# Optimization experiments

Hardware: AMD Instinct MI355X
Metric: run time of the kernel (lower is better)

Reference implementation:

```python
import jax, jax.numpy as jnp
import numpy as np

EMBED_DIM = 1024
BATCH, SEQ = 4, 2048


def setup_inputs() -> dict:
    key = jax.random.key(0)
    k1, k2 = jax.random.split(key)
    hidden_states = jax.random.normal(k1, (BATCH, SEQ, EMBED_DIM), dtype=jnp.float32)
    # fused QKV projection weight (Linear(embed_dim, 3*embed_dim, bias=False)),
    # stored as [E, 3E] so y = x @ W
    W_qkv = jax.random.normal(k2, (EMBED_DIM, 3 * EMBED_DIM), dtype=jnp.float32) * (1.0 / np.sqrt(EMBED_DIM))
    return {"hidden_states": hidden_states, "W_qkv": W_qkv}


def reference(hidden_states, W_qkv):
    E = hidden_states.shape[-1]
    scale = 1.0 / np.sqrt(E)
    qkv = jnp.einsum('bse,ef->bsf', hidden_states, W_qkv)  # [B,S,3E]
    q, k, v = jnp.split(qkv, 3, axis=-1)                   # each [B,S,E]
    # scores = q @ (k^T * scale); softmax over keys
    scores = jnp.einsum('bqe,bke->bqk', q, k) * scale      # [B,S,S]
    w = jax.nn.softmax(scores, axis=-1)
    return jnp.einsum('bqk,bke->bqe', w, v)                # [B,S,E]
```

## Files before the change

### kernel.cpp

```cpp
#include <hip/hip_runtime.h>

typedef __attribute__((ext_vector_type(8))) short short8;
typedef __attribute__((ext_vector_type(8))) unsigned short ushort8;
typedef __attribute__((ext_vector_type(4))) float f32x4;

__device__ __forceinline__ float bf2f(unsigned short u) {
  union { unsigned int u; float f; } c; c.u = ((unsigned int)u) << 16; return c.f;
}
__device__ __forceinline__ unsigned short f2bf(float f) {
  union { float f; unsigned int u; } c; c.f = f;
  unsigned int x = c.u;
  return (unsigned short)((x + 0x7FFFu + ((x >> 16) & 1u)) >> 16);
}

#define GLD_LDS16(g, l)                                                        \
  __builtin_amdgcn_global_load_lds(                                            \
      (const __attribute__((address_space(1))) void*)(g),                      \
      (__attribute__((address_space(3))) void*)(l), 16, 0, 0)

__global__ __launch_bounds__(256) void prep_kernel(
    const float* __restrict__ X, unsigned short* __restrict__ Xb,
    const float* __restrict__ W, unsigned short* __restrict__ Wt,
    float* __restrict__ Lrow) {
  const int t = threadIdx.x;
  if (blockIdx.x < 4096) {
    long i = ((long)blockIdx.x * 256 + t) * 8;
    float4 a = *(const float4*)(X + i);
    float4 b = *(const float4*)(X + i + 4);
    ushort8 o;
    o[0] = f2bf(a.x); o[1] = f2bf(a.y); o[2] = f2bf(a.z); o[3] = f2bf(a.w);
    o[4] = f2bf(b.x); o[5] = f2bf(b.y); o[6] = f2bf(b.z); o[7] = f2bf(b.w);
    *(ushort8*)(Xb + i) = o;
  } else if (blockIdx.x < 4864) {
    const int bid = blockIdx.x - 4096;
    const int f0 = (bid % 48) * 64;
    const int e0 = (bid / 48) * 64;
    __shared__ unsigned short tile[64][65];
    const int cg = (t & 15) * 4;
    const int r = t >> 4;
#pragma unroll
    for (int i = 0; i < 4; ++i) {
      int e = r + i * 16;
      float4 v = *(const float4*)(W + (long)(e0 + e) * 3072 + f0 + cg);
      tile[e][cg + 0] = f2bf(v.x);
      tile[e][cg + 1] = f2bf(v.y);
      tile[e][cg + 2] = f2bf(v.z);
      tile[e][cg + 3] = f2bf(v.w);
    }
    __syncthreads();
#pragma unroll
    for (int i = 0; i < 4; ++i) {
      int f = (t >> 4) + i * 16;
      int e = (t & 15) * 4;
      ushort4 o;
      o.x = tile[e + 0][f];
      o.y = tile[e + 1][f];
      o.z = tile[e + 2][f];
      o.w = tile[e + 3][f];
      *(ushort4*)(Wt + (long)(f0 + f) * 1024 + e0 + e) = o;
    }
  } else {
    float4 z = {0.f, 0.f, 0.f, 0.f};
#pragma unroll
    for (int j = 0; j < 8; ++j) *(float4*)(Lrow + (j * 256 + t) * 4) = z;
  }
}

template <int MODE>
__device__ __forceinline__ void gemm_body(
    const unsigned short* __restrict__ A, const unsigned short* __restrict__ B,
    void* __restrict__ Cv, int K, int lda, int ldb, int ldc,
    long sA, long sB, long sC, float alpha, float* __restrict__ Lrow,
    unsigned short* __restrict__ Vt) {
  constexpr int BM = 128, BN = 128, BK = 64;
  __shared__ __align__(16) unsigned short smem[BM * BK + BN * BK];
  unsigned short* As = smem;
  unsigned short* Bs = smem + BM * BK;

  const int t = threadIdx.x;
  const int lane = t & 63;
  const int wave = t >> 6;
  const int quad = lane >> 4;
  const int mrow = lane & 15;
  const int wm = wave >> 1, wn = wave & 1;

  const int bx = blockIdx.x, by = blockIdx.y;
  const int rowA0 = by * BM;
  const int rowB0 = bx * BN;
  const int b = blockIdx.z;
  const unsigned short* Ab = A + (long)b * sA;
  const unsigned short* Bb = B + (long)b * sB;

  f32x4 acc[4][4];
#pragma unroll
  for (int i = 0; i < 4; ++i)
#pragma unroll
    for (int j = 0; j < 4; ++j) {
      f32x4 z = {0.f, 0.f, 0.f, 0.f};
      acc[i][j] = z;
    }

  const int rbase = wave * 32 + (lane >> 3);
  const int c2 = lane & 7;

  for (int kt = 0; kt < K; kt += BK) {
#pragma unroll
    for (int j = 0; j < 4; ++j) {
      int r = rbase + j * 8;
      int c = c2 ^ (r & 7);
      GLD_LDS16(Ab + (long)(rowA0 + r) * lda + kt + c * 8, As + (wave * 4 + j) * 512);
      GLD_LDS16(Bb + (long)(rowB0 + r) * ldb + kt + c * 8, Bs + (wave * 4 + j) * 512);
    }
    __syncthreads();
#pragma unroll
    for (int ks = 0; ks < 2; ++ks) {
      short8 af[4], bfr[4];
#pragma unroll
      for (int i = 0; i < 4; ++i) {
        int rA = wm * 64 + i * 16 + mrow;
        int cc = ks * 4 + quad;
        af[i] = *(const short8*)(As + (rA * 8 + (cc ^ (rA & 7))) * 8);
        int rB = wn * 64 + i * 16 + mrow;
        bfr[i] = *(const short8*)(Bs + (rB * 8 + (cc ^ (rB & 7))) * 8);
      }
#pragma unroll
      for (int mt = 0; mt < 4; ++mt)
#pragma unroll
        for (int nt = 0; nt < 4; ++nt)
          acc[mt][nt] = __builtin_amdgcn_mfma_f32_16x16x32_bf16(
              af[mt], bfr[nt], acc[mt][nt], 0, 0, 0);
    }
    __syncthreads();
  }

  const int m_base = rowA0 + wm * 64;
  const int n_base = rowB0 + wn * 64;
  const long cb = (long)b * sC;

  if constexpr (MODE == 0) {
    if (bx < 16) {
#pragma unroll
      for (int mt = 0; mt < 4; ++mt)
#pragma unroll
        for (int nt = 0; nt < 4; ++nt)
#pragma unroll
          for (int i = 0; i < 4; ++i) {
            int row = m_base + mt * 16 + quad * 4 + i;
            int col = n_base + nt * 16 + mrow;
            ((unsigned short*)Cv)[cb + (long)row * ldc + col] = f2bf(acc[mt][nt][i]);
          }
    } else {
#pragma unroll
      for (int mt = 0; mt < 4; ++mt)
#pragma unroll
        for (int nt = 0; nt < 4; ++nt) {
          int r4 = wm * 64 + mt * 16 + quad * 4;
          int cL = wn * 64 + nt * 16 + mrow;
          int swz = ((cL & 7) << 4) ^ (((cL >> 3) & 3) << 3);
          ushort4 pk;
          pk.x = f2bf(acc[mt][nt][0]);
          pk.y = f2bf(acc[mt][nt][1]);
          pk.z = f2bf(acc[mt][nt][2]);
          pk.w = f2bf(acc[mt][nt][3]);
          *(ushort4*)(smem + cL * 128 + (r4 ^ swz)) = pk;
        }
      __syncthreads();
      const int batch = by >> 4;
      const int s_base = (by & 15) * 128;
      const int e_base = (bx - 16) * 128;
      unsigned short* VtB = Vt + (long)batch * 1024 * 2048;
#pragma unroll
      for (int rnd = 0; rnd < 8; ++rnd) {
        int e = (t >> 4) + rnd * 16;
        int s = (t & 15) * 8;
        int swz = ((e & 7) << 4) ^ (((e >> 3) & 3) << 3);
        ushort8 v = *(const ushort8*)(smem + e * 128 + (s ^ swz));
        *(ushort8*)(VtB + (long)(e_base + e) * 2048 + s_base + s) = v;
      }
    }
  } else if constexpr (MODE == 1) {
    float p[4][4];
#pragma unroll
    for (int mt = 0; mt < 4; ++mt)
#pragma unroll
      for (int i = 0; i < 4; ++i) p[mt][i] = 0.f;
#pragma unroll
    for (int mt = 0; mt < 4; ++mt)
#pragma unroll
      for (int nt = 0; nt < 4; ++nt)
#pragma unroll
        for (int i = 0; i < 4; ++i) {
          int row = m_base + mt * 16 + quad * 4 + i;
          int col = n_base + nt * 16 + mrow;
          float e = __expf(acc[mt][nt][i] * alpha);
          ((unsigned short*)Cv)[cb + (long)row * ldc + col] = f2bf(e);
          p[mt][i] += e;
        }
#pragma unroll
    for (int off = 1; off < 16; off <<= 1)
#pragma unroll
      for (int mt = 0; mt < 4; ++mt)
#pragma unroll
        for (int i = 0; i < 4; ++i)
          p[mt][i] += __shfl_xor(p[mt][i], off, 64);
    if (mrow == 0) {
#pragma unroll
      for (int mt = 0; mt < 4; ++mt)
#pragma unroll
        for (int i = 0; i < 4; ++i) {
          int row = m_base + mt * 16 + quad * 4 + i;
          atomicAdd(&Lrow[b * 2048 + row], p[mt][i]);
        }
    }
  } else {
#pragma unroll
    for (int mt = 0; mt < 4; ++mt)
#pragma unroll
      for (int i = 0; i < 4; ++i) {
        int row = m_base + mt * 16 + quad * 4 + i;
        float inv = 1.0f / Lrow[b * 2048 + row];
#pragma unroll
        for (int nt = 0; nt < 4; ++nt) {
          int col = n_base + nt * 16 + mrow;
          ((float*)Cv)[cb + (long)row * ldc + col] = acc[mt][nt][i] * inv;
        }
      }
  }
}

__global__ __launch_bounds__(256, 2) void qkv_gemm_kernel(
    const unsigned short* __restrict__ A, const unsigned short* __restrict__ B,
    void* __restrict__ Cv, int K, int lda, int ldb, int ldc,
    long sA, long sB, long sC, float alpha, float* __restrict__ Lrow,
    unsigned short* __restrict__ Vt) {
  gemm_body<0>(A, B, Cv, K, lda, ldb, ldc, sA, sB, sC, alpha, Lrow, Vt);
}
__global__ __launch_bounds__(256, 2) void score_gemm_kernel(
    const unsigned short* __restrict__ A, const unsigned short* __restrict__ B,
    void* __restrict__ Cv, int K, int lda, int ldb, int ldc,
    long sA, long sB, long sC, float alpha, float* __restrict__ Lrow,
    unsigned short* __restrict__ Vt) {
  gemm_body<1>(A, B, Cv, K, lda, ldb, ldc, sA, sB, sC, alpha, Lrow, Vt);
}
__global__ __launch_bounds__(256, 2) void out_gemm_kernel(
    const unsigned short* __restrict__ A, const unsigned short* __restrict__ B,
    void* __restrict__ Cv, int K, int lda, int ldb, int ldc,
    long sA, long sB, long sC, float alpha, float* __restrict__ Lrow,
    unsigned short* __restrict__ Vt) {
  gemm_body<2>(A, B, Cv, K, lda, ldb, ldc, sA, sB, sC, alpha, Lrow, Vt);
}

extern "C" void kernel_launch(void* const* d_in, const int* in_sizes, int n_in,
                              void* d_out, int out_size, void* d_ws, size_t ws_size,
                              hipStream_t stream) {
  const float* X = (const float*)d_in[0];
  const float* W = (const float*)d_in[1];
  float* out = (float*)d_out;

  char* ws = (char*)d_ws;
  unsigned short* Xb  = (unsigned short*)(ws);
  unsigned short* Wtb = (unsigned short*)(ws + 16777216);
  unsigned short* QK  = (unsigned short*)(ws + 23068672);
  unsigned short* Vt  = (unsigned short*)(ws + 56623104);
  unsigned short* Sb  = (unsigned short*)(ws + 73400320);
  float* Lrow         = (float*)(ws + 106954752);

  prep_kernel<<<4865, 256, 0, stream>>>(X, Xb, W, Wtb, Lrow);

  qkv_gemm_kernel<<<dim3(24, 64, 1), 256, 0, stream>>>(
      Xb, Wtb, QK, 1024, 1024, 1024, 2048, 0L, 0L, 0L, 1.0f, nullptr, Vt);

  score_gemm_kernel<<<dim3(16, 16, 4), 256, 0, stream>>>(
      QK, QK + 1024, Sb, 1024, 2048, 2048, 2048,
      (long)2048 * 2048, (long)2048 * 2048, (long)2048 * 2048, 0.03125f, Lrow, nullptr);

  out_gemm_kernel<<<dim3(8, 16, 4), 256, 0, stream>>>(
      Sb, Vt, out, 2048, 2048, 2048, 1024,
      (long)2048 * 2048, (long)1024 * 2048, (long)2048 * 1024, 1.0f, Lrow, nullptr);
}
```

Baseline: 228.8 us.

## Add 256x256-tile 8-wave pipelined GEMM for QKV and score kernels

Introduces a new GEMM body with 256x256 output tiles, 512 threads (8 waves), a double-buffered LDS pipeline of direct global-to-LDS loads split into half-K phases, raw barriers, and setprio around MFMA bursts. The QKV projection and score GEMMs switch to this body with smaller grids; the output GEMM keeps the old 128x128 body. The larger tiles raise data reuse and cut global traffic, and the interleaved loads try to hide memory latency behind MFMAs. In exchange it uses 128KB of LDS and many accumulator registers per block, so occupancy drops and the score grid becomes only 256 blocks, which may underfill the GPU.

```diff
diff --git a/kernel.cpp b/kernel.cpp
--- a/kernel.cpp
+++ b/kernel.cpp
@@ -17,6 +17,12 @@
   __builtin_amdgcn_global_load_lds(                                            \
       (const __attribute__((address_space(1))) void*)(g),                      \
       (__attribute__((address_space(3))) void*)(l), 16, 0, 0)
+
+__device__ __forceinline__ void bar() {
+  asm volatile("" ::: "memory");
+  __builtin_amdgcn_s_barrier();
+  asm volatile("" ::: "memory");
+}
 
 __global__ __launch_bounds__(256) void prep_kernel(
     const float* __restrict__ X, unsigned short* __restrict__ Xb,
@@ -67,6 +73,242 @@
 }
 
 template <int MODE>
+__device__ __forceinline__ void gemm256_body(
+    const unsigned short* __restrict__ A, const unsigned short* __restrict__ B,
+    void* __restrict__ Cv, int K, int lda, int ldb, int ldc,
+    long sA, long sB, long sC, float alpha, float* __restrict__ Lrow,
+    unsigned short* __restrict__ Vt) {
+  __shared__ __align__(16) unsigned short smem[65536];
+
+  const int t = threadIdx.x;
+  const int lane = t & 63;
+  const int wave = t >> 6;
+  const int quad = lane >> 4;
+  const int mrow = lane & 15;
+  const int wm = wave >> 2;
+  const int wn = wave & 3;
+
+  const int bx = blockIdx.x, by = blockIdx.y, b = blockIdx.z;
+  const int rowA0 = by * 256;
+  const int rowB0 = bx * 256;
+  const unsigned short* Ab = A + (long)b * sA;
+  const unsigned short* Bb = B + (long)b * sB;
+
+  const int srow = lane >> 2;
+  const int schunk = (lane & 3) * 8;
+
+  f32x4 acc[8][4];
+#pragma unroll
+  for (int i = 0; i < 8; ++i)
+#pragma unroll
+    for (int j = 0; j < 4; ++j) {
+      f32x4 z = {0.f, 0.f, 0.f, 0.f};
+      acc[i][j] = z;
+    }
+
+  const int NT = K >> 6;
+
+  auto stg = [&](const unsigned short* gb, int ld, int r0, int kt, int kh,
+                 int roff) {
+#pragma unroll
+    for (int j = 0; j < 2; ++j)
+      GLD_LDS16(gb + (long)(r0 + j * 128 + wave * 16 + srow) * ld + kt +
+                    kh * 32 + schunk,
+                smem + roff + (j * 128 + wave * 16) * 32);
+  };
+
+  stg(Ab, lda, rowA0, 0, 0, 0);
+  stg(Bb, ldb, rowB0, 0, 0, 16384);
+  stg(Ab, lda, rowA0, 0, 1, 8192);
+  stg(Bb, ldb, rowB0, 0, 1, 24576);
+  stg(Bb, ldb, rowB0, 64, 0, 32768 + 16384);
+  stg(Ab, lda, rowA0, 64, 0, 32768);
+  asm volatile("s_waitcnt vmcnt(4)" ::: "memory");
+  bar();
+
+  const int rA_base = wm * 128 + mrow;
+  const int rB_base = wn * 64 + mrow;
+  const int qoff = quad * 8;
+
+  for (int T = 0; T < NT; ++T) {
+    const int buf = (T & 1) << 15;
+    const int nbuf = buf ^ 32768;
+    const unsigned short* A0 = smem + buf;
+    const unsigned short* A1 = smem + buf + 8192;
+    const unsigned short* B0 = smem + buf + 16384;
+    const unsigned short* B1 = smem + buf + 24576;
+    const int ktn = (T + 1) << 6;
+    const int ktn2 = (T + 2) << 6;
+    short8 af[4], bf[4];
+
+#pragma unroll
+    for (int i = 0; i < 4; ++i)
+      af[i] = *(const short8*)(A0 + (rA_base + i * 16) * 32 + qoff);
+#pragma unroll
+    for (int j = 0; j < 4; ++j)
+      bf[j] = *(const short8*)(B0 + (rB_base + j * 16) * 32 + qoff);
+    if (T + 1 < NT) stg(Ab, lda, rowA0, ktn, 1, nbuf + 8192);
+    bar();
+    __builtin_amdgcn_sched_barrier(0);
+    __builtin_amdgcn_s_setprio(1);
+#pragma unroll
+    for (int i = 0; i < 4; ++i)
+#pragma unroll
+      for (int j = 0; j < 4; ++j)
+        acc[i][j] = __builtin_amdgcn_mfma_f32_16x16x32_bf16(af[i], bf[j],
+                                                            acc[i][j], 0, 0, 0);
+    __builtin_amdgcn_s_setprio(0);
+    __builtin_amdgcn_sched_barrier(0);
+    bar();
+
+#pragma unroll
+    for (int i = 0; i < 4; ++i)
+      af[i] = *(const short8*)(A0 + (rA_base + 64 + i * 16) * 32 + qoff);
+    if (T + 1 < NT) stg(Bb, ldb, rowB0, ktn, 1, nbuf + 24576);
+    bar();
+    __builtin_amdgcn_sched_barrier(0);
+    __builtin_amdgcn_s_setprio(1);
+#pragma unroll
+    for (int i = 0; i < 4; ++i)
+#pragma unroll
+      for (int j = 0; j < 4; ++j)
+        acc[4 + i][j] = __builtin_amdgcn_mfma_f32_16x16x32_bf16(
+            af[i], bf[j], acc[4 + i][j], 0, 0, 0);
+    __builtin_amdgcn_s_setprio(0);
+    __builtin_amdgcn_sched_barrier(0);
+    bar();
+
+#pragma unroll
+    for (int i = 0; i < 4; ++i)
+      af[i] = *(const short8*)(A1 + (rA_base + i * 16) * 32 + qoff);
+#pragma unroll
+    for (int j = 0; j < 4; ++j)
+      bf[j] = *(const short8*)(B1 + (rB_base + j * 16) * 32 + qoff);
+    if (T + 2 < NT) stg(Bb, ldb, rowB0, ktn2, 0, buf + 16384);
+    bar();
+    __builtin_amdgcn_sched_barrier(0);
+    __builtin_amdgcn_s_setprio(1);
+#pragma unroll
+    for (int i = 0; i < 4; ++i)
+#pragma unroll
+      for (int j = 0; j < 4; ++j)
+        acc[i][j] = __builtin_amdgcn_mfma_f32_16x16x32_bf16(af[i], bf[j],
+                                                            acc[i][j], 0, 0, 0);
+    __builtin_amdgcn_s_setprio(0);
+    __builtin_amdgcn_sched_barrier(0);
+    bar();
+
+#pragma unroll
+    for (int i = 0; i < 4; ++i)
+      af[i] = *(const short8*)(A1 + (rA_base + 64 + i * 16) * 32 + qoff);
+    if (T + 2 < NT) stg(Ab, lda, rowA0, ktn2, 0, buf);
+    bar();
+    __builtin_amdgcn_sched_barrier(0);
+    __builtin_amdgcn_s_setprio(1);
+#pragma unroll
+    for (int i = 0; i < 4; ++i)
+#pragma unroll
+      for (int j = 0; j < 4; ++j)
+        acc[4 + i][j] = __builtin_amdgcn_mfma_f32_16x16x32_bf16(
+            af[i], bf[j], acc[4 + i][j], 0, 0, 0);
+    __builtin_amdgcn_s_setprio(0);
+    __builtin_amdgcn_sched_barrier(0);
+    if (T + 2 < NT) {
+      asm volatile("s_waitcnt vmcnt(4)" ::: "memory");
+    } else if (T + 1 < NT) {
+      asm volatile("s_waitcnt vmcnt(0)" ::: "memory");
+    }
+    bar();
+  }
+
+  const long cb = (long)b * sC;
+
+  if constexpr (MODE == 0) {
+    if (bx < 8) {
+      unsigned short* C = (unsigned short*)Cv;
+#pragma unroll
+      for (int m = 0; m < 8; ++m) {
+        int row = rowA0 + wm * 128 + m * 16 + quad * 4;
+#pragma unroll
+        for (int j = 0; j < 4; ++j) {
+          int col = rowB0 + wn * 64 + j * 16 + mrow;
+#pragma unroll
+          for (int r = 0; r < 4; ++r)
+            C[(long)(row + r) * ldc + col] = f2bf(acc[m][j][r]);
+        }
+      }
+    } else {
+#pragma unroll
+      for (int m = 0; m < 8; ++m) {
+        int s4 = wm * 128 + m * 16 + quad * 4;
+#pragma unroll
+        for (int j = 0; j < 4; ++j) {
+          int e = wn * 64 + j * 16 + mrow;
+          int swz = ((e & 7) << 4) ^ (((e >> 3) & 3) << 3);
+          ushort4 pk;
+          pk.x = f2bf(acc[m][j][0]);
+          pk.y = f2bf(acc[m][j][1]);
+          pk.z = f2bf(acc[m][j][2]);
+          pk.w = f2bf(acc[m][j][3]);
+          *(ushort4*)(smem + e * 256 + (s4 ^ swz)) = pk;
+        }
+      }
+      __syncthreads();
+      const int batch = by >> 3;
+      const int s_base = (by & 7) * 256;
+      const int e_base = (bx - 8) * 256;
+      unsigned short* VtB = Vt + (long)batch * 1024 * 2048;
+      const int er = t >> 5;
+      const int s = (t & 31) * 8;
+#pragma unroll
+      for (int rnd = 0; rnd < 16; ++rnd) {
+        int e = rnd * 16 + er;
+        int swz = ((e & 7) << 4) ^ (((e >> 3) & 3) << 3);
+        ushort8 v = *(const ushort8*)(smem + e * 256 + (s ^ swz));
+        *(ushort8*)(VtB + (long)(e_base + e) * 2048 + s_base + s) = v;
+      }
+    }
+  } else {
+    unsigned short* C = (unsigned short*)Cv;
+    float p[8][4];
+#pragma unroll
+    for (int m = 0; m < 8; ++m)
+#pragma unroll
+      for (int r = 0; r < 4; ++r) p[m][r] = 0.f;
+#pragma unroll
+    for (int m = 0; m < 8; ++m) {
+      int row = rowA0 + wm * 128 + m * 16 + quad * 4;
+#pragma unroll
+      for (int j = 0; j < 4; ++j) {
+        int col = rowB0 + wn * 64 + j * 16 + mrow;
+#pragma unroll
+        for (int r = 0; r < 4; ++r) {
+          float e = __expf(acc[m][j][r] * alpha);
+          C[cb + (long)(row + r) * ldc + col] = f2bf(e);
+          p[m][r] += e;
+        }
+      }
+    }
+#pragma unroll
+    for (int off = 1; off < 16; off <<= 1)
+#pragma unroll
+      for (int m = 0; m < 8; ++m)
+#pragma unroll
+        for (int r = 0; r < 4; ++r)
+          p[m][r] += __shfl_xor(p[m][r], off, 64);
+    if (mrow == 0) {
+#pragma unroll
+      for (int m = 0; m < 8; ++m) {
+        int row = rowA0 + wm * 128 + m * 16 + quad * 4;
+#pragma unroll
+        for (int r = 0; r < 4; ++r)
+          atomicAdd(&Lrow[b * 2048 + row + r], p[m][r]);
+      }
+    }
+  }
+}
+
+template <int MODE>
 __device__ __forceinline__ void gemm_body(
     const unsigned short* __restrict__ A, const unsigned short* __restrict__ B,
     void* __restrict__ Cv, int K, int lda, int ldb, int ldc,
@@ -137,110 +379,33 @@
   const int n_base = rowB0 + wn * 64;
   const long cb = (long)b * sC;
 
-  if constexpr (MODE == 0) {
-    if (bx < 16) {
-#pragma unroll
-      for (int mt = 0; mt < 4; ++mt)
-#pragma unroll
-        for (int nt = 0; nt < 4; ++nt)
-#pragma unroll
-          for (int i = 0; i < 4; ++i) {
-            int row = m_base + mt * 16 + quad * 4 + i;
-            int col = n_base + nt * 16 + mrow;
-            ((unsigned short*)Cv)[cb + (long)row * ldc + col] = f2bf(acc[mt][nt][i]);
-          }
-    } else {
-#pragma unroll
-      for (int mt = 0; mt < 4; ++mt)
-#pragma unroll
-        for (int nt = 0; nt < 4; ++nt) {
-          int r4 = wm * 64 + mt * 16 + quad * 4;
-          int cL = wn * 64 + nt * 16 + mrow;
-          int swz = ((cL & 7) << 4) ^ (((cL >> 3) & 3) << 3);
-          ushort4 pk;
-          pk.x = f2bf(acc[mt][nt][0]);
-          pk.y = f2bf(acc[mt][nt][1]);
-          pk.z = f2bf(acc[mt][nt][2]);
-          pk.w = f2bf(acc[mt][nt][3]);
-          *(ushort4*)(smem + cL * 128 + (r4 ^ swz)) = pk;
-        }
-      __syncthreads();
-      const int batch = by >> 4;
-      const int s_base = (by & 15) * 128;
-      const int e_base = (bx - 16) * 128;
-      unsigned short* VtB = Vt + (long)batch * 1024 * 2048;
-#pragma unroll
-      for (int rnd = 0; rnd < 8; ++rnd) {
-        int e = (t >> 4) + rnd * 16;
-        int s = (t & 15) * 8;
-        int swz = ((e & 7) << 4) ^ (((e >> 3) & 3) << 3);
-        ushort8 v = *(const ushort8*)(smem + e * 128 + (s ^ swz));
-        *(ushort8*)(VtB + (long)(e_base + e) * 2048 + s_base + s) = v;
-      }
-    }
-  } else if constexpr (MODE == 1) {
-    float p[4][4];
-#pragma unroll
-    for (int mt = 0; mt < 4; ++mt)
-#pragma unroll
-      for (int i = 0; i < 4; ++i) p[mt][i] = 0.f;
-#pragma unroll
-    for (int mt = 0; mt < 4; ++mt)
-#pragma unroll
-      for (int nt = 0; nt < 4; ++nt)
-#pragma unroll
-        for (int i = 0; i < 4; ++i) {
-          int row = m_base + mt * 16 + quad * 4 + i;
-          int col = n_base + nt * 16 + mrow;
-          float e = __expf(acc[mt][nt][i] * alpha);
-          ((unsigned short*)Cv)[cb + (long)row * ldc + col] = f2bf(e);
-          p[mt][i] += e;
-        }
-#pragma unroll
-    for (int off = 1; off < 16; off <<= 1)
-#pragma unroll
-      for (int mt = 0; mt < 4; ++mt)
-#pragma unroll
-        for (int i = 0; i < 4; ++i)
-          p[mt][i] += __shfl_xor(p[mt][i], off, 64);
-    if (mrow == 0) {
-#pragma unroll
-      for (int mt = 0; mt < 4; ++mt)
-#pragma unroll
-        for (int i = 0; i < 4; ++i) {
-          int row = m_base + mt * 16 + quad * 4 + i;
-          atomicAdd(&Lrow[b * 2048 + row], p[mt][i]);
-        }
-    }
-  } else {
-#pragma unroll
-    for (int mt = 0; mt < 4; ++mt)
-#pragma unroll
-      for (int i = 0; i < 4; ++i) {
-        int row = m_base + mt * 16 + quad * 4 + i;
-        float inv = 1.0f / Lrow[b * 2048 + row];
-#pragma unroll
-        for (int nt = 0; nt < 4; ++nt) {
-          int col = n_base + nt * 16 + mrow;
-          ((float*)Cv)[cb + (long)row * ldc + col] = acc[mt][nt][i] * inv;
-        }
-      }
-  }
-}
-
-__global__ __launch_bounds__(256, 2) void qkv_gemm_kernel(
+#pragma unroll
+  for (int mt = 0; mt < 4; ++mt)
+#pragma unroll
+    for (int i = 0; i < 4; ++i) {
+      int row = m_base + mt * 16 + quad * 4 + i;
+      float inv = 1.0f / Lrow[b * 2048 + row];
+#pragma unroll
+      for (int nt = 0; nt < 4; ++nt) {
+        int col = n_base + nt * 16 + mrow;
+        ((float*)Cv)[cb + (long)row * ldc + col] = acc[mt][nt][i] * inv;
+      }
+    }
+}
+
+__global__ __launch_bounds__(512, 2) void qkv_gemm_kernel(
     const unsigned short* __restrict__ A, const unsigned short* __restrict__ B,
     void* __restrict__ Cv, int K, int lda, int ldb, int ldc,
     long sA, long sB, long sC, float alpha, float* __restrict__ Lrow,
     unsigned short* __restrict__ Vt) {
-  gemm_body<0>(A, B, Cv, K, lda, ldb, ldc, sA, sB, sC, alpha, Lrow, Vt);
-}
-__global__ __launch_bounds__(256, 2) void score_gemm_kernel(
+  gemm256_body<0>(A, B, Cv, K, lda, ldb, ldc, sA, sB, sC, alpha, Lrow, Vt);
+}
+__global__ __launch_bounds__(512, 2) void score_gemm_kernel(
     const unsigned short* __restrict__ A, const unsigned short* __restrict__ B,
     void* __restrict__ Cv, int K, int lda, int ldb, int ldc,
     long sA, long sB, long sC, float alpha, float* __restrict__ Lrow,
     unsigned short* __restrict__ Vt) {
-  gemm_body<1>(A, B, Cv, K, lda, ldb, ldc, sA, sB, sC, alpha, Lrow, Vt);
+  gemm256_body<1>(A, B, Cv, K, lda, ldb, ldc, sA, sB, sC, alpha, Lrow, Vt);
 }
 __global__ __launch_bounds__(256, 2) void out_gemm_kernel(
     const unsigned short* __restrict__ A, const unsigned short* __restrict__ B,
@@ -267,10 +432,10 @@
 
   prep_kernel<<<4865, 256, 0, stream>>>(X, Xb, W, Wtb, Lrow);
 
-  qkv_gemm_kernel<<<dim3(24, 64, 1), 256, 0, stream>>>(
+  qkv_gemm_kernel<<<dim3(12, 32, 1), 512, 0, stream>>>(
       Xb, Wtb, QK, 1024, 1024, 1024, 2048, 0L, 0L, 0L, 1.0f, nullptr, Vt);
 
-  score_gemm_kernel<<<dim3(16, 16, 4), 256, 0, stream>>>(
+  score_gemm_kernel<<<dim3(8, 8, 4), 512, 0, stream>>>(
       QK, QK + 1024, Sb, 1024, 2048, 2048, 2048,
       (long)2048 * 2048, (long)2048 * 2048, (long)2048 * 2048, 0.03125f, Lrow, nullptr);
 
```

Result: slower. 250.1 us (+9.3%).
